# Kernel tuning notes

Measured on AMD Instinct MI355X. Metric: run time of the kernel, lower is better.

## Reference

```python
import jax, jax.numpy as jnp
import numpy as np

B, P, M, W = 32, 4096, 12, 9
IN_C, OUT_C = 64, 64
IN_PN_PAD = P + 1  # in_point_num + 1 padding row


def setup_inputs() -> dict:
    key = jax.random.key(0)
    k1, k2, k3, k4 = jax.random.split(key, 4)
    in_pc_pad = jax.random.normal(k1, (B, IN_PN_PAD, IN_C), dtype=jnp.float32)
    weights = jax.random.normal(k2, (W, OUT_C * IN_C), dtype=jnp.float32)
    bias = jnp.zeros((OUT_C,), dtype=jnp.float32)
    w_weights = jax.random.normal(k3, (P, M, W), dtype=jnp.float32) / (9.0 * W)
    neighbor_id_lstlst = jax.random.randint(k4, (P, M), 0, IN_PN_PAD, dtype=jnp.int64)
    neighbor_mask_lst = jnp.ones((P, M), dtype=jnp.float32)
    return {
        "in_pc_pad": in_pc_pad,
        "weights": weights,
        "bias": bias,
        "w_weights": w_weights,
        "neighbor_id_lstlst": neighbor_id_lstlst,
        "neighbor_mask_lst": neighbor_mask_lst,
    }


def reference(in_pc_pad, weights, bias, w_weights, neighbor_id_lstlst, neighbor_mask_lst):
    # gather neighbor features: [B, P, M, IN_C]
    in_neighbors = in_pc_pad[:, neighbor_id_lstlst]
    # mask the per-(point,neighbor) basis coefficients: [P, M, W]
    w2 = w_weights * neighbor_mask_lst[:, :, None]
    # synthesize per-(point,neighbor) weight matrices from basis: [P, M, OUT_C, IN_C]
    wmat = jnp.einsum('pmw,wc->pmc', w2, weights).reshape(P, M, OUT_C, IN_C)
    # batched matvec + neighbor-sum reduce (fused over m): [B, P, OUT_C]
    out_pc = jnp.einsum('pmoi,bpmi->bpo', wmat, in_neighbors)
    return out_pc + bias
```

## Files before the change

kernel.cpp:

```cpp
#include <hip/hip_runtime.h>

#define NB 32
#define NP 4096
#define NM 12
#define NW 9
#define NC 64
#define PN_PAD 4097
#define KDIM (NW * NC)
#define NKS (KDIM / 16)
#define AROW 584

#define WSW_BYTES (KDIM * NC * 2)
#define W2_OFFSET WSW_BYTES
#define W2_BYTES (NP * NM * 12 * 4)
#define XB_OFFSET (W2_OFFSET + W2_BYTES)
#define XB_BYTES (NB * PN_PAD * NC * 2)
#define WS_NEED ((size_t)XB_OFFSET + XB_BYTES)

typedef __attribute__((ext_vector_type(8))) short short8;
typedef __attribute__((ext_vector_type(2))) float float2v;
typedef __attribute__((ext_vector_type(4))) float float4v;
typedef __attribute__((ext_vector_type(16))) float float16v;

__device__ __forceinline__ unsigned short f32_to_bf16(float f) {
    union { float f; unsigned u; } v; v.f = f;
    unsigned r = v.u + 0x7FFFu + ((v.u >> 16) & 1u);
    return (unsigned short)(r >> 16);
}

__device__ __forceinline__ uint2 pack_bf16x4(float4v v) {
    union { float f; unsigned u; } a0, a1, a2, a3;
    a0.f = v[0]; a1.f = v[1]; a2.f = v[2]; a3.f = v[3];
    unsigned u0 = a0.u + 0x8000u, u1 = a1.u + 0x8000u;
    unsigned u2 = a2.u + 0x8000u, u3 = a3.u + 0x8000u;
    uint2 r;
    r.x = __builtin_amdgcn_perm(u1, u0, 0x07060302u);
    r.y = __builtin_amdgcn_perm(u3, u2, 0x07060302u);
    return r;
}

__device__ __forceinline__ uint2 pack_bf16x4_2(float2v lo, float2v hi) {
    union { float f; unsigned u; } a0, a1, a2, a3;
    a0.f = lo[0]; a1.f = lo[1]; a2.f = hi[0]; a3.f = hi[1];
    unsigned u0 = a0.u + 0x8000u, u1 = a1.u + 0x8000u;
    unsigned u2 = a2.u + 0x8000u, u3 = a3.u + 0x8000u;
    uint2 r;
    r.x = __builtin_amdgcn_perm(u1, u0, 0x07060302u);
    r.y = __builtin_amdgcn_perm(u3, u2, 0x07060302u);
    return r;
}

__device__ __forceinline__ void bf16x4_to_2xf2(uint2 u, float2v& lo, float2v& hi) {
    union { unsigned u; float f; } c0, c1, c2, c3;
    c0.u = u.x << 16; c1.u = u.x & 0xFFFF0000u;
    c2.u = u.y << 16; c3.u = u.y & 0xFFFF0000u;
    lo = (float2v){c0.f, c1.f};
    hi = (float2v){c2.f, c3.f};
}

template<int DOX>
__global__ void prep_all(const float* __restrict__ w,
                         const float* __restrict__ ww,
                         const float* __restrict__ mask,
                         const float* __restrict__ x,
                         unsigned short* __restrict__ wsw,
                         float* __restrict__ w2d,
                         unsigned short* __restrict__ xb) {
    int idx = blockIdx.x * 256 + threadIdx.x;
    if (idx < KDIM * NC) {
        int j    = idx & 7;
        int lane = (idx >> 3) & 63;
        int f    = idx >> 9;
        int nt2  = f & 1;
        int ks   = f >> 1;
        int k = ks * 16 + ((lane >> 5) * 8) + j;
        int n = nt2 * 32 + (lane & 31);
        int wi = k >> 6;
        int ii = k & 63;
        wsw[idx] = f32_to_bf16(w[wi * (NC * NC) + n * NC + ii]);
    }
    if (idx < NP * NM * NW) {
        int wq = idx % NW;
        int pm = idx / NW;
        w2d[pm * 12 + wq] = ww[idx] * mask[pm];
    }
    if (DOX) {
        const int n4 = NB * PN_PAD * NC / 4;
        if (idx < n4) {
            const float4v* x4 = (const float4v*)x;
            ((uint2*)xb)[idx] = pack_bf16x4(x4[idx]);
        }
    }
}

template<int BF16X>
__global__ __launch_bounds__(512)
void conv_main(const float* __restrict__ x,
               const unsigned short* __restrict__ xb,
               const unsigned short* __restrict__ wsw,
               const float* __restrict__ bias,
               const float* __restrict__ w2d,
               const int* __restrict__ nid,
               float* __restrict__ out) {
    __shared__ __align__(16) unsigned short A[NB * AROW];

    const int p = blockIdx.x;
    const int tid = threadIdx.x;

    {
        const int i4 = tid & 15;
        const int b  = tid >> 4;
        const float* w2p = w2d + p * (NM * 12);
        const int* nidp = nid + p * NM;

        int nm[NM];
        #pragma unroll
        for (int m = 0; m < NM; ++m) nm[m] = nidp[m];

        float2v acc0[NW], acc1[NW];
        #pragma unroll
        for (int w = 0; w < NW; ++w) {
            acc0[w] = (float2v){0.f, 0.f};
            acc1[w] = (float2v){0.f, 0.f};
        }

        if (BF16X) {
            const uint2* xb2 = (const uint2*)xb;
            uint2 xv[NM];
            #pragma unroll
            for (int m = 0; m < NM; ++m)
                xv[m] = xb2[(b * PN_PAD + nm[m]) * 16 + i4];
            #pragma unroll
            for (int m = 0; m < NM; ++m) {
                float2v lo, hi;
                bf16x4_to_2xf2(xv[m], lo, hi);
                #pragma unroll
                for (int w = 0; w < NW; ++w) {
                    const float ws = w2p[m * 12 + w];
                    acc0[w] += lo * ws;
                    acc1[w] += hi * ws;
                }
            }
        } else {
            const float4v* x4 = (const float4v*)x;
            float4v xv[NM];
            #pragma unroll
            for (int m = 0; m < NM; ++m)
                xv[m] = x4[(b * PN_PAD + nm[m]) * 16 + i4];
            #pragma unroll
            for (int m = 0; m < NM; ++m) {
                const float2v lo = {xv[m][0], xv[m][1]};
                const float2v hi = {xv[m][2], xv[m][3]};
                #pragma unroll
                for (int w = 0; w < NW; ++w) {
                    const float ws = w2p[m * 12 + w];
                    acc0[w] += lo * ws;
                    acc1[w] += hi * ws;
                }
            }
        }

        #pragma unroll
        for (int w = 0; w < NW; ++w)
            *(uint2*)&A[b * AROW + w * 64 + i4 * 4] = pack_bf16x4_2(acc0[w], acc1[w]);
    }
    __syncthreads();

    {
        const int lane = tid & 63;
        const int wid  = tid >> 6;
        if (wid < 2) {
            const int col  = lane & 31;
            const int half = lane >> 5;
            float16v acc = {0.f,0.f,0.f,0.f, 0.f,0.f,0.f,0.f,
                            0.f,0.f,0.f,0.f, 0.f,0.f,0.f,0.f};
            const short8* Bfrags = (const short8*)wsw;

            #pragma unroll
            for (int ks = 0; ks < NKS; ++ks) {
                short8 bfrag = Bfrags[(ks * 2 + wid) * 64 + lane];
                const short8 a = *(const short8*)&A[col * AROW + ks * 16 + half * 8];
                acc = __builtin_amdgcn_mfma_f32_32x32x16_bf16(a, bfrag, acc, 0, 0, 0);
            }

            const int o = wid * 32 + col;
            const float bv = bias[o];
            #pragma unroll
            for (int reg = 0; reg < 16; ++reg) {
                const int b = (reg & 3) + 8 * (reg >> 2) + 4 * half;
                out[(b * NP + p) * NC + o] = acc[reg] + bv;
            }
        }
    }
}

extern "C" void kernel_launch(void* const* d_in, const int* in_sizes, int n_in,
                              void* d_out, int out_size, void* d_ws, size_t ws_size,
                              hipStream_t stream) {
    const float* x    = (const float*)d_in[0];
    const float* w    = (const float*)d_in[1];
    const float* bias = (const float*)d_in[2];
    const float* ww   = (const float*)d_in[3];
    const int*   nid  = (const int*)d_in[4];
    const float* mask = (const float*)d_in[5];
    float* out = (float*)d_out;
    unsigned short* wsw = (unsigned short*)d_ws;
    float* w2d = (float*)((char*)d_ws + W2_OFFSET);
    unsigned short* xb = (unsigned short*)((char*)d_ws + XB_OFFSET);

    if (ws_size >= WS_NEED) {
        const int n4 = NB * PN_PAD * NC / 4;
        hipLaunchKernelGGL(prep_all<1>, dim3((n4 + 255) / 256), dim3(256), 0, stream,
                           w, ww, mask, x, wsw, w2d, xb);
        hipLaunchKernelGGL(conv_main<1>, dim3(NP), dim3(512), 0, stream,
                           x, xb, wsw, bias, w2d, nid, out);
    } else {
        const int prep_elems = NP * NM * NW;
        hipLaunchKernelGGL(prep_all<0>, dim3((prep_elems + 255) / 256), dim3(256), 0, stream,
                           w, ww, mask, x, wsw, w2d, xb);
        hipLaunchKernelGGL(conv_main<0>, dim3(NP), dim3(512), 0, stream,
                           x, xb, wsw, bias, w2d, nid, out);
    }
}
```

Measured before the change: 131.0 us.

## Split MFMA K-loop across all eight waves and use packed FMA asm

Previously only two of eight waves ran the MFMA K-loop. Now each wave handles one N-tile and one K-chunk, writes its partial accumulators to shared memory, and a cross-wave reduction adds the bias and writes the output. The per-neighbor basis FMA also switches to inline v_pk_fma_f32 with paired weight loads, which needs the w2d padding slots zero-filled. This costs two extra barriers and a shared-memory round trip for the partial sums. The "s" constraint on per-thread loaded weights may force readfirstlane or fail to compile.

```diff
diff --git a/kernel.cpp b/kernel.cpp
--- a/kernel.cpp
+++ b/kernel.cpp
@@ -8,6 +8,8 @@
 #define PN_PAD 4097
 #define KDIM (NW * NC)
 #define NKS (KDIM / 16)
+#define KCH 4
+#define KSPC (NKS / KCH)
 #define AROW 584
 
 #define WSW_BYTES (KDIM * NC * 2)
@@ -21,6 +23,13 @@
 typedef __attribute__((ext_vector_type(2))) float float2v;
 typedef __attribute__((ext_vector_type(4))) float float4v;
 typedef __attribute__((ext_vector_type(16))) float float16v;
+
+#define PK_FMA_LO(acc, x, wp)                                                  \
+    asm("v_pk_fma_f32 %0, %1, %2, %0 op_sel:[0,0,0] op_sel_hi:[1,0,1]"         \
+        : "+v"(acc) : "v"(x), "s"(wp))
+#define PK_FMA_HI(acc, x, wp)                                                  \
+    asm("v_pk_fma_f32 %0, %1, %2, %0 op_sel:[0,1,0] op_sel_hi:[1,1,1]"         \
+        : "+v"(acc) : "v"(x), "s"(wp))
 
 __device__ __forceinline__ unsigned short f32_to_bf16(float f) {
     union { float f; unsigned u; } v; v.f = f;
@@ -79,10 +88,12 @@
         int ii = k & 63;
         wsw[idx] = f32_to_bf16(w[wi * (NC * NC) + n * NC + ii]);
     }
-    if (idx < NP * NM * NW) {
-        int wq = idx % NW;
-        int pm = idx / NW;
-        w2d[pm * 12 + wq] = ww[idx] * mask[pm];
+    if (idx < NP * NM * 12) {
+        int wq = idx % 12;
+        int pm = idx / 12;
+        float v = 0.f;
+        if (wq < NW) v = ww[pm * NW + wq] * mask[pm];
+        w2d[idx] = v;
     }
     if (DOX) {
         const int n4 = NB * PN_PAD * NC / 4;
@@ -110,7 +121,7 @@
     {
         const int i4 = tid & 15;
         const int b  = tid >> 4;
-        const float* w2p = w2d + p * (NM * 12);
+        const float2v* w2pv = (const float2v*)(w2d + p * (NM * 12));
         const int* nidp = nid + p * NM;
 
         int nm[NM];
@@ -135,11 +146,16 @@
                 float2v lo, hi;
                 bf16x4_to_2xf2(xv[m], lo, hi);
                 #pragma unroll
-                for (int w = 0; w < NW; ++w) {
-                    const float ws = w2p[m * 12 + w];
-                    acc0[w] += lo * ws;
-                    acc1[w] += hi * ws;
+                for (int j = 0; j < 4; ++j) {
+                    const float2v wp = w2pv[m * 6 + j];
+                    PK_FMA_LO(acc0[2 * j],     lo, wp);
+                    PK_FMA_LO(acc1[2 * j],     hi, wp);
+                    PK_FMA_HI(acc0[2 * j + 1], lo, wp);
+                    PK_FMA_HI(acc1[2 * j + 1], hi, wp);
                 }
+                const float2v wp8 = w2pv[m * 6 + 4];
+                PK_FMA_LO(acc0[8], lo, wp8);
+                PK_FMA_LO(acc1[8], hi, wp8);
             }
         } else {
             const float4v* x4 = (const float4v*)x;
@@ -152,11 +168,16 @@
                 const float2v lo = {xv[m][0], xv[m][1]};
                 const float2v hi = {xv[m][2], xv[m][3]};
                 #pragma unroll
-                for (int w = 0; w < NW; ++w) {
-                    const float ws = w2p[m * 12 + w];
-                    acc0[w] += lo * ws;
-                    acc1[w] += hi * ws;
+                for (int j = 0; j < 4; ++j) {
+                    const float2v wp = w2pv[m * 6 + j];
+                    PK_FMA_LO(acc0[2 * j],     lo, wp);
+                    PK_FMA_LO(acc1[2 * j],     hi, wp);
+                    PK_FMA_HI(acc0[2 * j + 1], lo, wp);
+                    PK_FMA_HI(acc1[2 * j + 1], hi, wp);
                 }
+                const float2v wp8 = w2pv[m * 6 + 4];
+                PK_FMA_LO(acc0[8], lo, wp8);
+                PK_FMA_LO(acc1[8], hi, wp8);
             }
         }
 
@@ -169,27 +190,45 @@
     {
         const int lane = tid & 63;
         const int wid  = tid >> 6;
-        if (wid < 2) {
-            const int col  = lane & 31;
-            const int half = lane >> 5;
-            float16v acc = {0.f,0.f,0.f,0.f, 0.f,0.f,0.f,0.f,
-                            0.f,0.f,0.f,0.f, 0.f,0.f,0.f,0.f};
-            const short8* Bfrags = (const short8*)wsw;
-
-            #pragma unroll
-            for (int ks = 0; ks < NKS; ++ks) {
-                short8 bfrag = Bfrags[(ks * 2 + wid) * 64 + lane];
-                const short8 a = *(const short8*)&A[col * AROW + ks * 16 + half * 8];
-                acc = __builtin_amdgcn_mfma_f32_32x32x16_bf16(a, bfrag, acc, 0, 0, 0);
-            }
-
-            const int o = wid * 32 + col;
-            const float bv = bias[o];
-            #pragma unroll
-            for (int reg = 0; reg < 16; ++reg) {
-                const int b = (reg & 3) + 8 * (reg >> 2) + 4 * half;
-                out[(b * NP + p) * NC + o] = acc[reg] + bv;
-            }
+        const int nt   = wid & 1;
+        const int kc   = wid >> 1;
+        const int col  = lane & 31;
+        const int hf   = lane >> 5;
+
+        float16v acc = {0.f,0.f,0.f,0.f, 0.f,0.f,0.f,0.f,
+                        0.f,0.f,0.f,0.f, 0.f,0.f,0.f,0.f};
+        const short8* Bfrags = (const short8*)wsw;
+
+        #pragma unroll
+        for (int s = 0; s < KSPC; ++s) {
+            const int ks = kc * KSPC + s;
+            short8 bfrag = Bfrags[(ks * 2 + nt) * 64 + lane];
+            const short8 a = *(const short8*)&A[col * AROW + ks * 16 + hf * 8];
+            acc = __builtin_amdgcn_mfma_f32_32x32x16_bf16(a, bfrag, acc, 0, 0, 0);
+        }
+        __syncthreads();
+
+        float* P = (float*)A;
+        #pragma unroll
+        for (int reg = 0; reg < 16; ++reg) {
+            const int row = (reg & 3) + 8 * (reg >> 2) + 4 * hf;
+            P[((nt * KCH + kc) * 32 + row) * 32 + col] = acc[reg];
+        }
+        __syncthreads();
+
+        const int c  = tid & 31;
+        const int rg = (tid >> 5) & 7;
+        const int t2 = tid >> 8;
+        const int o  = t2 * 32 + c;
+        const float bv = bias[o];
+        #pragma unroll
+        for (int rr = 0; rr < 4; ++rr) {
+            const int r = rg * 4 + rr;
+            const float s = P[((t2 * KCH + 0) * 32 + r) * 32 + c]
+                          + P[((t2 * KCH + 1) * 32 + r) * 32 + c]
+                          + P[((t2 * KCH + 2) * 32 + r) * 32 + c]
+                          + P[((t2 * KCH + 3) * 32 + r) * 32 + c];
+            out[(r * NP + p) * NC + o] = s + bv;
         }
     }
 }
@@ -215,7 +254,7 @@
         hipLaunchKernelGGL(conv_main<1>, dim3(NP), dim3(512), 0, stream,
                            x, xb, wsw, bias, w2d, nid, out);
     } else {
-        const int prep_elems = NP * NM * NW;
+        const int prep_elems = NP * NM * 12;
         hipLaunchKernelGGL(prep_all<0>, dim3((prep_elems + 255) / 256), dim3(256), 0, stream,
                            w, ww, mask, x, wsw, w2d, xb);
         hipLaunchKernelGGL(conv_main<0>, dim3(NP), dim3(512), 0, stream,
```

Result: no change. 132.5 us (+1.1%).
